# Performance work log

Hardware: AMD Instinct MI355X
Metric: run time of the kernel (lower is better)

The kernel has to match this reference:

```python
import jax, jax.numpy as jnp
import numpy as np

B, PANO, OBJ, CFG, LM, IMG, D = 64, 36, 36, 16, 8, 32, 300
H, EMB, ANG, FEAT = 512, 64, 128, 2176
TOPN = 3
EPS = 1e-8


def setup_inputs() -> dict:
    key = jax.random.key(0)
    ks = jax.random.split(key, 24)
    f = lambda i, shape: jax.random.normal(ks[i], shape, dtype=jnp.float32)
    u = lambda i, shape: jax.random.uniform(ks[i], shape, dtype=jnp.float32)
    s = 0.02
    return {
        "action": f(0, (B, ANG)),
        "feature": f(1, (B, PANO, FEAT)),
        "cand_feat": f(2, (B, IMG, FEAT)),
        "prev_h1": f(3, (B, H)),
        "c_0": f(4, (B, H)),
        "ctx": f(5, (B, CFG, H)),
        "s_0": u(6, (B, CFG)),
        "landmark_object_feature": f(7, (B, CFG, LM, D)),
        "candidate_obj_text_feat": f(8, (B, IMG, OBJ, D)),
        "landmark_mask": u(9, (B, CFG, LM)),
        "landmark_relation": f(10, (B, CFG, LM, 6)),
        "landmark_relation_mask": u(11, (B, CFG, LM)),
        "candidate_relation": f(12, (B, IMG, 6)),
        "pano_obj_feat": f(13, (B, PANO, OBJ, D)),
        "emb_W": f(14, (ANG, EMB)) * s,
        "emb_b": jnp.zeros((EMB,), jnp.float32),
        "W_ih": f(15, (EMB + FEAT + TOPN * D, 4 * H)) * s,
        "W_hh": f(16, (H, 4 * H)) * s,
        "b_lstm": jnp.zeros((4 * H,), jnp.float32),
        "feat_in_W": f(17, (H, FEAT + TOPN * D)) * s,
        "att_in_W": f(18, (H, H)) * s,
        "att_out_W": f(19, (2 * H, H)) * s,
        "cand_in_W": f(20, (H, FEAT + TOPN * 7 + TOPN * D)) * s,
        "ctx_mask": jnp.zeros((B, CFG), dtype=bool),
    }


def _cos_argmax(obj_feat, land_flat):
    # obj_feat: [B,I,O,D], land_flat: [B,M,D] -> argmax over O of cosine sim: [B,I,M]
    dot = jnp.einsum('biod,bmd->biom', obj_feat, land_flat)
    na = jnp.linalg.norm(obj_feat, axis=-1)
    nb = jnp.linalg.norm(land_flat, axis=-1)
    sim = dot / jnp.maximum(na[..., None] * nb[:, None, None, :], EPS)
    return jnp.argmax(sim, axis=2)


def reference(action, feature, cand_feat, prev_h1, c_0, ctx, s_0,
              landmark_object_feature, candidate_obj_text_feat, landmark_mask,
              landmark_relation, landmark_relation_mask, candidate_relation,
              pano_obj_feat, emb_W, emb_b, W_ih, W_hh, b_lstm, feat_in_W,
              att_in_W, att_out_W, cand_in_W, ctx_mask):
    M = CFG * LM
    land_flat = landmark_object_feature.reshape(B, M, D)

    # --- pano object retrieval (cosine argmax + top-N config*landmark gather) ---
    pano_idx = _cos_argmax(pano_obj_feat, land_flat)                   # [B,36,M]
    top_idx = jax.lax.top_k((s_0[..., None] * landmark_mask).reshape(B, M), TOPN)[1]  # [B,3]
    sel = jnp.take_along_axis(pano_idx, jnp.broadcast_to(top_idx[:, None, :], (B, PANO, TOPN)), axis=2)
    pano_sim_obj = jnp.take_along_axis(
        pano_obj_feat, jnp.broadcast_to(sel[..., None], (B, PANO, TOPN, D)), axis=2
    ).reshape(B, PANO, TOPN * D)

    # --- embed action, feature attention (dropout = identity in eval) ---
    action_embeds = jnp.tanh(action @ emb_W + emb_b)
    feat_all = jnp.concatenate([feature, pano_sim_obj], axis=-1)       # [B,36,FEAT+900]
    a = jnp.einsum('bsd,bd->bs', feat_all, prev_h1 @ feat_in_W)
    p = jax.nn.softmax(a, axis=-1)
    attn_feat = jnp.einsum('bs,bsd->bd', p, feat_all)

    # --- LSTM cell ---
    gates = jnp.concatenate([action_embeds, attn_feat], axis=-1) @ W_ih + prev_h1 @ W_hh + b_lstm
    i_g, f_g, g_g, o_g = jnp.split(gates, 4, axis=-1)
    c_1 = jax.nn.sigmoid(f_g) * c_0 + jax.nn.sigmoid(i_g) * jnp.tanh(g_g)
    h_1 = jax.nn.sigmoid(o_g) * jnp.tanh(c_1)

    # --- ctx attention with mask + tilde ---
    lg = jnp.einsum('bsd,bd->bs', ctx, h_1 @ att_in_W)
    lg = jnp.where(ctx_mask, -jnp.inf, lg)
    ctx_attn = jax.nn.softmax(lg, axis=-1)
    wctx = jnp.einsum('bs,bsd->bd', ctx_attn, ctx)
    h_tilde = jnp.tanh(jnp.concatenate([wctx, h_1], axis=-1) @ att_out_W)

    # --- candidate object retrieval ---
    cand_idx = _cos_argmax(candidate_obj_text_feat, land_flat)         # [B,IMG,M]
    ctop = jax.lax.top_k((ctx_attn[..., None] * landmark_mask).reshape(B, M), TOPN)[1]
    land_rel_top = jnp.take_along_axis(landmark_relation.reshape(B, M, 6),
                                       jnp.broadcast_to(ctop[..., None], (B, TOPN, 6)), axis=1)
    land_obj_rel = jnp.einsum('bik,bjk->bij', candidate_relation, land_rel_top)   # [B,IMG,3]
    rel_mask_top = jnp.take_along_axis(landmark_relation_mask.reshape(B, M), ctop, axis=1)  # [B,3]
    csel = jnp.take_along_axis(cand_idx, jnp.broadcast_to(ctop[:, None, :], (B, IMG, TOPN)), axis=2)
    candi_sim_obj = jnp.take_along_axis(
        candidate_obj_text_feat, jnp.broadcast_to(csel[..., None], (B, IMG, TOPN, D)), axis=2)
    candi_rel = candidate_relation[:, :, None, :] * rel_mask_top[:, None, :, None]  # [B,IMG,3,6]
    new_feat = jnp.concatenate(
        [candi_sim_obj, jnp.concatenate([candi_rel, land_obj_rel[..., None]], axis=-1)],
        axis=-1).reshape(B, IMG, TOPN * (D + 7))
    cand_all = jnp.concatenate([cand_feat, new_feat], axis=-1)

    logit = jnp.einsum('bsd,bd->bs', cand_all, h_tilde @ cand_in_W)
    return h_1, c_1, logit, h_tilde, ctx_attn
```

## Files before the change

kernel.cpp:

```cpp
#include <hip/hip_runtime.h>
#include <math.h>

#define B_    64
#define PANO_ 36
#define OBJ_  36
#define CFG_  16
#define LM_   8
#define IMG_  32
#define D_    300
#define H_    512
#define EMB_  64
#define ANG_  128
#define FEAT_ 2176
#define M_    128

__device__ __forceinline__ float sigmoidf(float x) { return 1.0f / (1.0f + expf(-x)); }
__device__ __forceinline__ float dot4(float4 a, float4 b) {
    return a.x * b.x + a.y * b.y + a.z * b.z + a.w * b.w;
}

template <int TWO_SEG>
__global__ __launch_bounds__(256)
void gemm_part(const float* __restrict__ A0, int lda0, int K0, const float* __restrict__ W0,
               const float* __restrict__ A1, int lda1, int K1, const float* __restrict__ W1,
               float* __restrict__ part, int N, int kchunk) {
    __shared__ __align__(16) float As[64][36];
    __shared__ __align__(16) float Bs[32][68];
    const int K = K0 + (TWO_SEG ? K1 : 0);
    int n0 = blockIdx.x * 64;
    int k0 = blockIdx.y * kchunk;
    if (k0 >= K) return;
    int kend = min(K, k0 + kchunk);
    int tid = threadIdx.x;
    int tr = tid >> 4, tc = tid & 15;
    float rA[8], rB[8];
    float acc[4][4] = {};

    auto loadA = [&](int kb) {
#pragma unroll
        for (int l = 0; l < 8; l++) {
            int idx = tid + 256 * l;
            int r = idx >> 5, kk = idx & 31, k = kb + kk;
            float v = 0.f;
            if (k < kend) {
                if (TWO_SEG && k >= K0) v = A1[(size_t)r * lda1 + (k - K0)];
                else                    v = A0[(size_t)r * lda0 + k];
            }
            rA[l] = v;
        }
    };
    auto loadB = [&](int kb) {
#pragma unroll
        for (int l = 0; l < 8; l++) {
            int idx = tid + 256 * l;
            int kk = idx >> 6, c = idx & 63;
            int k = kb + kk, n = n0 + c;
            float v = 0.f;
            if (k < kend && n < N) {
                if (TWO_SEG && k >= K0) v = W1[(size_t)(k - K0) * N + n];
                else                    v = W0[(size_t)k * N + n];
            }
            rB[l] = v;
        }
    };
    auto storeLDS = [&]() {
#pragma unroll
        for (int l = 0; l < 8; l++) {
            int idx = tid + 256 * l;
            As[idx >> 5][idx & 31] = rA[l];
            Bs[idx >> 6][idx & 63] = rB[l];
        }
    };
    auto compute = [&]() {
#pragma unroll
        for (int kk0 = 0; kk0 < 32; kk0 += 4) {
            float4 a0 = *reinterpret_cast<const float4*>(&As[4 * tr + 0][kk0]);
            float4 a1 = *reinterpret_cast<const float4*>(&As[4 * tr + 1][kk0]);
            float4 a2 = *reinterpret_cast<const float4*>(&As[4 * tr + 2][kk0]);
            float4 a3 = *reinterpret_cast<const float4*>(&As[4 * tr + 3][kk0]);
            float4 b0 = *reinterpret_cast<const float4*>(&Bs[kk0 + 0][4 * tc]);
            float4 b1 = *reinterpret_cast<const float4*>(&Bs[kk0 + 1][4 * tc]);
            float4 b2 = *reinterpret_cast<const float4*>(&Bs[kk0 + 2][4 * tc]);
            float4 b3 = *reinterpret_cast<const float4*>(&Bs[kk0 + 3][4 * tc]);
#define ROWFMA(i, ai) \
            acc[i][0] += ai.x * b0.x + ai.y * b1.x + ai.z * b2.x + ai.w * b3.x; \
            acc[i][1] += ai.x * b0.y + ai.y * b1.y + ai.z * b2.y + ai.w * b3.y; \
            acc[i][2] += ai.x * b0.z + ai.y * b1.z + ai.z * b2.z + ai.w * b3.z; \
            acc[i][3] += ai.x * b0.w + ai.y * b1.w + ai.z * b2.w + ai.w * b3.w;
            ROWFMA(0, a0) ROWFMA(1, a1) ROWFMA(2, a2) ROWFMA(3, a3)
#undef ROWFMA
        }
    };

    loadA(k0); loadB(k0);
    storeLDS();
    __syncthreads();
    for (int kb = k0 + 32; kb < kend; kb += 32) {
        loadA(kb); loadB(kb);
        compute();
        __syncthreads();
        storeLDS();
        __syncthreads();
    }
    compute();

    float* outp = part + (size_t)blockIdx.y * 64 * N;
#pragma unroll
    for (int i = 0; i < 4; i++) {
        int r = 4 * tr + i;
#pragma unroll
        for (int j = 0; j < 4; j++) {
            int n = n0 + 4 * tc + j;
            if (n < N) outp[(size_t)r * N + n] = acc[i][j];
        }
    }
}

__global__ void reduce_kernel(const float* __restrict__ part, int S, int total,
                              float* __restrict__ out) {
    int i = blockIdx.x * 256 + threadIdx.x;
    if (i >= total) return;
    float v = 0.f;
    for (int s = 0; s < S; s++) v += part[(size_t)s * total + i];
    out[i] = v;
}

__global__ void reduce_pad_kernel(const float* __restrict__ part, int S, int ncols,
                                  int ostride, float* __restrict__ out) {
    int b = blockIdx.y;
    int i = blockIdx.x * 256 + threadIdx.x;
    if (i >= ncols) return;
    float v = 0.f;
    for (int s = 0; s < S; s++) v += part[(size_t)s * (B_ * ncols) + (size_t)b * ncols + i];
    out[(size_t)b * ostride + i] = v;
}

__global__ void tanh_reduce_kernel(const float* __restrict__ part, int S,
                                   float* __restrict__ htld, float* __restrict__ out_ht) {
    int i = blockIdx.x * 256 + threadIdx.x;
    if (i >= B_ * H_) return;
    float v = 0.f;
    for (int s = 0; s < S; s++) v += part[(size_t)s * (B_ * H_) + i];
    float t = tanhf(v);
    htld[i] = t;
    out_ht[i] = t;
}

__global__ __launch_bounds__(256)
void pano_logits_kernel(const float* __restrict__ pobj,
                        const float* __restrict__ land,
                        const float* __restrict__ s0,
                        const float* __restrict__ lmask,
                        const float* __restrict__ feature,
                        const float* __restrict__ qfeat,
                        int* __restrict__ sel,
                        float* __restrict__ aval) {
    __shared__ __align__(16) float land3[3][304];
    __shared__ int mids[3];
    __shared__ float simv[3][40];
    __shared__ float redV[2];
    __shared__ int redI[2];
    __shared__ int fin[3];
    __shared__ float wred[4];
    int i = blockIdx.x, b = blockIdx.y, tid = threadIdx.x;
    int wave = tid >> 6, lane = tid & 63;

    float tv; int tm;
    if (tid < 128) { tv = s0[b * CFG_ + (tid >> 3)] * lmask[(size_t)b * M_ + tid]; tm = tid; }
    else { tv = -INFINITY; tm = 1 << 30; }
    for (int t = 0; t < 3; t++) {
        float bv = tv; int bi = tm;
        for (int off = 32; off >= 1; off >>= 1) {
            float ov = __shfl_xor(bv, off);
            int   oi = __shfl_xor(bi, off);
            if (ov > bv || (ov == bv && oi < bi)) { bv = ov; bi = oi; }
        }
        if (lane == 0 && wave < 2) { redV[wave] = bv; redI[wave] = bi; }
        __syncthreads();
        if (tid == 0)
            mids[t] = (redV[0] > redV[1] || (redV[0] == redV[1] && redI[0] < redI[1])) ? redI[0] : redI[1];
        __syncthreads();
        if (tm == mids[t]) tv = -INFINITY;
    }

    for (int idx = tid; idx < 912; idx += 256) {
        int t = idx / 304, k = idx % 304;
        land3[t][k] = (k < 300) ? land[((size_t)b * 128 + mids[t]) * 300 + k] : 0.f;
    }
    __syncthreads();

    int g = tid >> 2, gl = tid & 3;
    int o = (g < 36) ? g : 0;
    const float* obase = pobj + (((size_t)b * 36 + i) * 36) * 300;
    const float* row = obase + (size_t)o * 300;
    float c0 = 0, c1 = 0, c2 = 0, sn = 0;
    for (int k4 = gl; k4 < 75; k4 += 4) {
        float4 a  = *reinterpret_cast<const float4*>(row + 4 * k4);
        float4 l0 = *reinterpret_cast<const float4*>(&land3[0][4 * k4]);
        float4 l1 = *reinterpret_cast<const float4*>(&land3[1][4 * k4]);
        float4 l2 = *reinterpret_cast<const float4*>(&land3[2][4 * k4]);
        sn += dot4(a, a);
        c0 += dot4(a, l0);
        c1 += dot4(a, l1);
        c2 += dot4(a, l2);
    }
#pragma unroll
    for (int off = 1; off <= 2; off <<= 1) {
        c0 += __shfl_xor(c0, off);
        c1 += __shfl_xor(c1, off);
        c2 += __shfl_xor(c2, off);
        sn += __shfl_xor(sn, off);
    }
    if (gl == 0 && g < 36) {
        float inv = 1.0f / sqrtf(fmaxf(sn, 1e-20f));
        simv[0][g] = c0 * inv;
        simv[1][g] = c1 * inv;
        simv[2][g] = c2 * inv;
    }
    __syncthreads();
    if (tid < 3) {
        float bv = -INFINITY; int bo = 0;
        for (int o2 = 0; o2 < 36; o2++) {
            float v = simv[tid][o2];
            if (v > bv) { bv = v; bo = o2; }
        }
        fin[tid] = bo;
        sel[((size_t)b * 36 + i) * 3 + tid] = bo;
    }
    __syncthreads();

    const float* qf = qfeat + (size_t)b * 3076;
    const float* frow = feature + ((size_t)b * 36 + i) * 2176;
    float acc = 0;
    for (int d4 = tid; d4 < 544; d4 += 256)
        acc += dot4(*reinterpret_cast<const float4*>(frow + 4 * d4),
                    *reinterpret_cast<const float4*>(qf + 4 * d4));
    for (int idx = tid; idx < 225; idx += 256) {
        int t = idx / 75, k4 = idx % 75;
        acc += dot4(*reinterpret_cast<const float4*>(obase + (size_t)fin[t] * 300 + 4 * k4),
                    *reinterpret_cast<const float4*>(qf + 2176 + t * 300 + 4 * k4));
    }
    for (int off = 32; off >= 1; off >>= 1) acc += __shfl_xor(acc, off);
    if (lane == 0) wred[wave] = acc;
    __syncthreads();
    if (tid == 0) aval[b * 36 + i] = wred[0] + wred[1] + wred[2] + wred[3];
}

__global__ __launch_bounds__(256)
void attn_wsum_kernel(const float* __restrict__ feature,
                      const float* __restrict__ pobj,
                      const int* __restrict__ sel,
                      const float* __restrict__ aval,
                      const float* __restrict__ action,
                      const float* __restrict__ embW,
                      const float* __restrict__ embB,
                      float* __restrict__ xcat) {
    __shared__ float lg[36];
    __shared__ float pe[36];
    __shared__ int ss[36][3];
    int b = blockIdx.y, tid = threadIdx.x;
    int d = blockIdx.x * 256 + tid;
    if (tid < 36) lg[tid] = aval[b * 36 + tid];
    for (int idx = tid; idx < 108; idx += 256) ss[idx / 3][idx % 3] = sel[(size_t)b * 108 + idx];
    __syncthreads();
    float mx = -INFINITY;
    for (int s = 0; s < 36; s++) mx = fmaxf(mx, lg[s]);
    if (tid < 36) pe[tid] = expf(lg[tid] - mx);
    __syncthreads();
    float sum = 0;
    for (int s = 0; s < 36; s++) sum += pe[s];
    float invS = 1.0f / sum;
    if (d < 3076) {
        float acc = 0;
        if (d < 2176) {
            const float* fb = feature + (size_t)b * 36 * 2176 + d;
            for (int s = 0; s < 36; s++) acc += pe[s] * fb[(size_t)s * 2176];
        } else {
            int t = (d - 2176) / 300, k = (d - 2176) % 300;
            const float* pb = pobj + (size_t)b * 36 * 36 * 300;
            for (int s = 0; s < 36; s++)
                acc += pe[s] * pb[((size_t)s * 36 + ss[s][t]) * 300 + k];
        }
        xcat[(size_t)b * 3140 + 64 + d] = acc * invS;
    }
    if (blockIdx.x == 0 && tid < 64) {
        float acc = embB[tid];
        for (int k = 0; k < ANG_; k++)
            acc += action[b * ANG_ + k] * embW[k * EMB_ + tid];
        xcat[(size_t)b * 3140 + tid] = tanhf(acc);
    }
}

__global__ void lstm_kernel(const float* __restrict__ gp, int S,
                            const float* __restrict__ b_lstm,
                            const float* __restrict__ c0,
                            float* __restrict__ out_h1,
                            float* __restrict__ out_c1) {
    int idx = blockIdx.x * 256 + threadIdx.x;
    if (idx >= B_ * H_) return;
    int b = idx >> 9, d = idx & 511;
    float ig = b_lstm[d];
    float fg = b_lstm[512 + d];
    float gg = b_lstm[1024 + d];
    float og = b_lstm[1536 + d];
    for (int s = 0; s < S; s++) {
        const float* g = gp + (size_t)s * (B_ * 2048) + (size_t)b * 2048;
        ig += g[d];
        fg += g[512 + d];
        gg += g[1024 + d];
        og += g[1536 + d];
    }
    float c1 = sigmoidf(fg) * c0[idx] + sigmoidf(ig) * tanhf(gg);
    float h1 = sigmoidf(og) * tanhf(c1);
    out_c1[idx] = c1;
    out_h1[idx] = h1;
}

__global__ __launch_bounds__(256)
void ctx_attn_kernel(const float* __restrict__ ctx,
                     const float* __restrict__ qctx_part,
                     const float* __restrict__ h1f,
                     const float* __restrict__ lmask,
                     float* __restrict__ ccbuf,
                     float* __restrict__ out_attn,
                     int* __restrict__ ctop) {
    __shared__ float qc[512];
    __shared__ float part[16][17];
    __shared__ float lgv[16];
    __shared__ float att[16];
    __shared__ float redV[2];
    __shared__ int redI[2];
    __shared__ int mids[3];
    int b = blockIdx.x, tid = threadIdx.x;
    int wave = tid >> 6, lane = tid & 63;
    for (int idx = tid; idx < 512; idx += 256) {
        float v = 0.f;
#pragma unroll
        for (int s = 0; s < 8; s++) v += qctx_part[(size_t)s * (B_ * 512) + (size_t)b * 512 + idx];
        qc[idx] = v;
    }
    __syncthreads();
    int s = tid >> 4, l = tid & 15;
    float acc = 0;
    for (int d = l; d < 512; d += 16) acc += ctx[((size_t)b * 16 + s) * 512 + d] * qc[d];
    part[s][l] = acc;
    __syncthreads();
    if (tid < 16) {
        float sum = 0;
        for (int j = 0; j < 16; j++) sum += part[tid][j];
        lgv[tid] = sum;
    }
    __syncthreads();
    if (tid < 16) {
        float mx = -INFINITY;
        for (int j = 0; j < 16; j++) mx = fmaxf(mx, lgv[j]);
        att[tid] = expf(lgv[tid] - mx);
    }
    __syncthreads();
    float sum = 0;
    for (int j = 0; j < 16; j++) sum += att[j];
    float invS = 1.0f / sum;
    if (tid < 16) out_attn[b * 16 + tid] = att[tid] * invS;
    for (int d = tid; d < 512; d += 256) {
        float acc2 = 0;
        for (int sj = 0; sj < 16; sj++)
            acc2 += att[sj] * ctx[((size_t)b * 16 + sj) * 512 + d];
        ccbuf[(size_t)b * 1024 + d] = acc2 * invS;
        ccbuf[(size_t)b * 1024 + 512 + d] = h1f[(size_t)b * 512 + d];
    }
    float tv; int tm;
    if (tid < 128) { tv = att[tid >> 3] * lmask[(size_t)b * M_ + tid]; tm = tid; }
    else { tv = -INFINITY; tm = 1 << 30; }
    for (int t = 0; t < 3; t++) {
        float bv = tv; int bi = tm;
        for (int off = 32; off >= 1; off >>= 1) {
            float ov = __shfl_xor(bv, off);
            int   oi = __shfl_xor(bi, off);
            if (ov > bv || (ov == bv && oi < bi)) { bv = ov; bi = oi; }
        }
        if (lane == 0 && wave < 2) { redV[wave] = bv; redI[wave] = bi; }
        __syncthreads();
        if (tid == 0) {
            int pick = (redV[0] > redV[1] || (redV[0] == redV[1] && redI[0] < redI[1])) ? redI[0] : redI[1];
            mids[t] = pick;
            ctop[b * 3 + t] = pick;
        }
        __syncthreads();
        if (tm == mids[t]) tv = -INFINITY;
    }
}

__global__ __launch_bounds__(256)
void cand_fused_kernel(const float* __restrict__ cobj,
                       const float* __restrict__ land,
                       const int* __restrict__ ctop,
                       const float* __restrict__ landrel,
                       const float* __restrict__ lrmask,
                       const float* __restrict__ crel_g,
                       const float* __restrict__ cand_feat,
                       const float* __restrict__ qcand,
                       float* __restrict__ out_logit) {
    __shared__ __align__(16) float land3[3][304];
    __shared__ float relL[3][6];
    __shared__ float relM[3];
    __shared__ float crel[6];
    __shared__ int mids[3];
    __shared__ float simv[3][40];
    __shared__ int fin[3];
    __shared__ float wsum[4];
    int img = blockIdx.x, b = blockIdx.y, tid = threadIdx.x;
    int wave = tid >> 6, lane = tid & 63;
    if (tid < 3) mids[tid] = ctop[b * 3 + tid];
    __syncthreads();
    for (int idx = tid; idx < 912; idx += 256) {
        int t = idx / 304, k = idx % 304;
        land3[t][k] = (k < 300) ? land[((size_t)b * 128 + mids[t]) * 300 + k] : 0.f;
    }
    if (tid < 18) { int t = tid / 6, k = tid % 6; relL[t][k] = landrel[((size_t)b * 128 + mids[t]) * 6 + k]; }
    if (tid >= 32 && tid < 35) { int t = tid - 32; relM[t] = lrmask[(size_t)b * 128 + mids[t]]; }
    if (tid >= 64 && tid < 70) { crel[tid - 64] = crel_g[((size_t)b * 32 + img) * 6 + (tid - 64)]; }
    __syncthreads();

    int g = tid >> 2, gl = tid & 3;
    int o = (g < 36) ? g : 0;
    const float* obase = cobj + (((size_t)b * 32 + img) * 36) * 300;
    const float* row = obase + (size_t)o * 300;
    float c0 = 0, c1 = 0, c2 = 0, sn = 0;
    for (int k4 = gl; k4 < 75; k4 += 4) {
        float4 a  = *reinterpret_cast<const float4*>(row + 4 * k4);
        float4 l0 = *reinterpret_cast<const float4*>(&land3[0][4 * k4]);
        float4 l1 = *reinterpret_cast<const float4*>(&land3[1][4 * k4]);
        float4 l2 = *reinterpret_cast<const float4*>(&land3[2][4 * k4]);
        sn += dot4(a, a);
        c0 += dot4(a, l0);
        c1 += dot4(a, l1);
        c2 += dot4(a, l2);
    }
#pragma unroll
    for (int off = 1; off <= 2; off <<= 1) {
        c0 += __shfl_xor(c0, off);
        c1 += __shfl_xor(c1, off);
        c2 += __shfl_xor(c2, off);
        sn += __shfl_xor(sn, off);
    }
    if (gl == 0 && g < 36) {
        float inv = 1.0f / sqrtf(fmaxf(sn, 1e-20f));
        simv[0][g] = c0 * inv;
        simv[1][g] = c1 * inv;
        simv[2][g] = c2 * inv;
    }
    __syncthreads();
    if (tid < 3) {
        float bv = -INFINITY; int bo = 0;
        for (int o2 = 0; o2 < 36; o2++) {
            float v = simv[tid][o2];
            if (v > bv) { bv = v; bo = o2; }
        }
        fin[tid] = bo;
    }
    __syncthreads();

    const float* q = qcand + (size_t)b * 3104;
    const float* cf = cand_feat + ((size_t)b * 32 + img) * 2176;
    float acc = 0;
    for (int d4 = tid; d4 < 544; d4 += 256)
        acc += dot4(*reinterpret_cast<const float4*>(cf + 4 * d4),
                    *reinterpret_cast<const float4*>(q + 4 * d4));
    for (int idx = tid; idx < 900; idx += 256) {
        int t = idx / 300, k = idx % 300;
        acc += obase[(size_t)fin[t] * 300 + k] * q[2176 + t * 307 + k];
    }
    if (tid < 21) {
        int t = tid / 7, j = tid % 7;
        float val;
        if (j < 6) val = crel[j] * relM[t];
        else { val = 0; for (int k = 0; k < 6; k++) val += crel[k] * relL[t][k]; }
        acc += val * q[2176 + t * 307 + 300 + j];
    }
    for (int off = 32; off >= 1; off >>= 1) acc += __shfl_xor(acc, off);
    if (lane == 0) wsum[wave] = acc;
    __syncthreads();
    if (tid == 0) {
        out_logit[(size_t)b * 32 + img] = wsum[0] + wsum[1] + wsum[2] + wsum[3];
    }
}

extern "C" void kernel_launch(void* const* d_in, const int* in_sizes, int n_in,
                              void* d_out, int out_size, void* d_ws, size_t ws_size,
                              hipStream_t stream) {
    const float* action    = (const float*)d_in[0];
    const float* feature   = (const float*)d_in[1];
    const float* cand_feat = (const float*)d_in[2];
    const float* prev_h1   = (const float*)d_in[3];
    const float* c_0       = (const float*)d_in[4];
    const float* ctx       = (const float*)d_in[5];
    const float* s_0       = (const float*)d_in[6];
    const float* lobj      = (const float*)d_in[7];
    const float* cobj      = (const float*)d_in[8];
    const float* lmask     = (const float*)d_in[9];
    const float* lrel      = (const float*)d_in[10];
    const float* lrelmask  = (const float*)d_in[11];
    const float* crel      = (const float*)d_in[12];
    const float* pobj      = (const float*)d_in[13];
    const float* embW      = (const float*)d_in[14];
    const float* embB      = (const float*)d_in[15];
    const float* W_ih      = (const float*)d_in[16];
    const float* W_hh      = (const float*)d_in[17];
    const float* b_lstm    = (const float*)d_in[18];
    const float* feat_in_W = (const float*)d_in[19];
    const float* att_in_W  = (const float*)d_in[20];
    const float* att_out_W = (const float*)d_in[21];
    const float* cand_in_W = (const float*)d_in[22];

    float* ws = (float*)d_ws;
    float* gates_part = ws;
    float* qf_part    = gates_part + 2621440;
    float* q_feat     = qf_part + 1574912;
    float* qctx_part  = q_feat + 196864;
    float* htpre_part = qctx_part + 262144;
    float* htld       = htpre_part + 524288;
    float* qcand_part = htld + 32768;
    float* q_cand     = qcand_part + 1585664;
    float* xcat       = q_cand + 198656;
    float* ccbuf      = xcat + 200960;
    float* aval       = ccbuf + 65536;
    int*   ctop       = (int*)(aval + 2304);
    int*   sel        = ctop + 192;

    float* out       = (float*)d_out;
    float* out_h1    = out;
    float* out_c1    = out + 32768;
    float* out_logit = out + 65536;
    float* out_ht    = out + 67584;
    float* out_attn  = out + 100352;

    gemm_part<0><<<dim3(49, 8), 256, 0, stream>>>(prev_h1, H_, H_, feat_in_W,
                                                  nullptr, 0, 0, nullptr,
                                                  qf_part, 3076, 64);
    reduce_kernel<<<769, 256, 0, stream>>>(qf_part, 8, 196864, q_feat);

    pano_logits_kernel<<<dim3(PANO_, B_), 256, 0, stream>>>(pobj, lobj, s_0, lmask, feature, q_feat, sel, aval);

    attn_wsum_kernel<<<dim3(13, B_), 256, 0, stream>>>(feature, pobj, sel, aval, action, embW, embB, xcat);

    gemm_part<1><<<dim3(32, 20), 256, 0, stream>>>(xcat, 3140, 3140, W_ih,
                                                   prev_h1, H_, H_, W_hh,
                                                   gates_part, 2048, 192);
    lstm_kernel<<<128, 256, 0, stream>>>(gates_part, 20, b_lstm, c_0, out_h1, out_c1);

    gemm_part<0><<<dim3(8, 8), 256, 0, stream>>>(out_h1, H_, H_, att_in_W,
                                                 nullptr, 0, 0, nullptr,
                                                 qctx_part, H_, 64);
    ctx_attn_kernel<<<B_, 256, 0, stream>>>(ctx, qctx_part, out_h1, lmask, ccbuf, out_attn, ctop);

    gemm_part<0><<<dim3(8, 16), 256, 0, stream>>>(ccbuf, 1024, 1024, att_out_W,
                                                  nullptr, 0, 0, nullptr,
                                                  htpre_part, H_, 64);
    tanh_reduce_kernel<<<128, 256, 0, stream>>>(htpre_part, 16, htld, out_ht);

    gemm_part<0><<<dim3(49, 8), 256, 0, stream>>>(htld, H_, H_, cand_in_W,
                                                  nullptr, 0, 0, nullptr,
                                                  qcand_part, 3097, 64);
    reduce_pad_kernel<<<dim3(13, B_), 256, 0, stream>>>(qcand_part, 8, 3097, 3104, q_cand);

    cand_fused_kernel<<<dim3(IMG_, B_), 256, 0, stream>>>(cobj, lobj, ctop, lrel, lrelmask,
                                                          crel, cand_feat, q_cand, out_logit);
}
```

Before: 462.7 us.

## Vectorize GEMM tile loads, reductions, LSTM and overlap feature dot with cosine pass

Switches the split-K GEMM to float4 global loads and LDS stores for A, and for B when N is a multiple of 4. The reduce, tanh-reduce, LSTM and attention weighted-sum kernels now work on float4 with fewer threads. In pano_logits and cand_fused, 144 threads handle the cosine-similarity rows with a one-step register prefetch while the other 112 threads compute the feature dot product at the same time, instead of doing the two phases one after the other. q_cand is remapped to a 308-stride layout so the selected-object dot can use aligned float4 loads. The intent is to cut the number of memory instructions and hide latency, at the cost of lower thread-level parallelism in some kernels.

```diff
diff --git a/kernel.cpp b/kernel.cpp
--- a/kernel.cpp
+++ b/kernel.cpp
@@ -18,8 +18,15 @@
 __device__ __forceinline__ float dot4(float4 a, float4 b) {
     return a.x * b.x + a.y * b.y + a.z * b.z + a.w * b.w;
 }
-
-template <int TWO_SEG>
+__device__ __forceinline__ float4 add4(float4 a, float4 b) {
+    return make_float4(a.x + b.x, a.y + b.y, a.z + b.z, a.w + b.w);
+}
+__device__ __forceinline__ float4 fma4(float s, float4 a, float4 acc) {
+    return make_float4(acc.x + s * a.x, acc.y + s * a.y, acc.z + s * a.z, acc.w + s * a.w);
+}
+__device__ __forceinline__ float4 ld4(const float* p) { return *reinterpret_cast<const float4*>(p); }
+
+template <int TWO_SEG, int VEC_B>
 __global__ __launch_bounds__(256)
 void gemm_part(const float* __restrict__ A0, int lda0, int K0, const float* __restrict__ W0,
                const float* __restrict__ A1, int lda1, int K1, const float* __restrict__ W1,
@@ -33,55 +40,89 @@
     int kend = min(K, k0 + kchunk);
     int tid = threadIdx.x;
     int tr = tid >> 4, tc = tid & 15;
-    float rA[8], rB[8];
+    float4 rA4[2];
+    float4 rB4[2];
+    float rB[8];
     float acc[4][4] = {};
 
     auto loadA = [&](int kb) {
 #pragma unroll
-        for (int l = 0; l < 8; l++) {
+        for (int l = 0; l < 2; l++) {
             int idx = tid + 256 * l;
-            int r = idx >> 5, kk = idx & 31, k = kb + kk;
-            float v = 0.f;
+            int r = idx >> 3, kq = idx & 7;
+            int k = kb + 4 * kq;
+            float4 v = make_float4(0.f, 0.f, 0.f, 0.f);
             if (k < kend) {
-                if (TWO_SEG && k >= K0) v = A1[(size_t)r * lda1 + (k - K0)];
-                else                    v = A0[(size_t)r * lda0 + k];
+                const float* src = (TWO_SEG && k >= K0)
+                    ? A1 + (size_t)r * lda1 + (k - K0)
+                    : A0 + (size_t)r * lda0 + k;
+                v = ld4(src);
             }
-            rA[l] = v;
+            rA4[l] = v;
         }
     };
     auto loadB = [&](int kb) {
-#pragma unroll
-        for (int l = 0; l < 8; l++) {
-            int idx = tid + 256 * l;
-            int kk = idx >> 6, c = idx & 63;
-            int k = kb + kk, n = n0 + c;
-            float v = 0.f;
-            if (k < kend && n < N) {
-                if (TWO_SEG && k >= K0) v = W1[(size_t)(k - K0) * N + n];
-                else                    v = W0[(size_t)k * N + n];
+        if (VEC_B) {
+#pragma unroll
+            for (int l = 0; l < 2; l++) {
+                int idx = tid + 256 * l;
+                int kk = idx >> 4, c4 = idx & 15;
+                int k = kb + kk, n = n0 + 4 * c4;
+                float4 v = make_float4(0.f, 0.f, 0.f, 0.f);
+                if (k < kend && n < N) {
+                    const float* src = (TWO_SEG && k >= K0)
+                        ? W1 + (size_t)(k - K0) * N + n
+                        : W0 + (size_t)k * N + n;
+                    v = ld4(src);
+                }
+                rB4[l] = v;
             }
-            rB[l] = v;
+        } else {
+#pragma unroll
+            for (int l = 0; l < 8; l++) {
+                int idx = tid + 256 * l;
+                int kk = idx >> 6, c = idx & 63;
+                int k = kb + kk, n = n0 + c;
+                float v = 0.f;
+                if (k < kend && n < N) {
+                    v = (TWO_SEG && k >= K0) ? W1[(size_t)(k - K0) * N + n]
+                                             : W0[(size_t)k * N + n];
+                }
+                rB[l] = v;
+            }
         }
     };
     auto storeLDS = [&]() {
 #pragma unroll
-        for (int l = 0; l < 8; l++) {
+        for (int l = 0; l < 2; l++) {
             int idx = tid + 256 * l;
-            As[idx >> 5][idx & 31] = rA[l];
-            Bs[idx >> 6][idx & 63] = rB[l];
+            *reinterpret_cast<float4*>(&As[idx >> 3][4 * (idx & 7)]) = rA4[l];
+        }
+        if (VEC_B) {
+#pragma unroll
+            for (int l = 0; l < 2; l++) {
+                int idx = tid + 256 * l;
+                *reinterpret_cast<float4*>(&Bs[idx >> 4][4 * (idx & 15)]) = rB4[l];
+            }
+        } else {
+#pragma unroll
+            for (int l = 0; l < 8; l++) {
+                int idx = tid + 256 * l;
+                Bs[idx >> 6][idx & 63] = rB[l];
+            }
         }
     };
     auto compute = [&]() {
 #pragma unroll
         for (int kk0 = 0; kk0 < 32; kk0 += 4) {
-            float4 a0 = *reinterpret_cast<const float4*>(&As[4 * tr + 0][kk0]);
-            float4 a1 = *reinterpret_cast<const float4*>(&As[4 * tr + 1][kk0]);
-            float4 a2 = *reinterpret_cast<const float4*>(&As[4 * tr + 2][kk0]);
-            float4 a3 = *reinterpret_cast<const float4*>(&As[4 * tr + 3][kk0]);
-            float4 b0 = *reinterpret_cast<const float4*>(&Bs[kk0 + 0][4 * tc]);
-            float4 b1 = *reinterpret_cast<const float4*>(&Bs[kk0 + 1][4 * tc]);
-            float4 b2 = *reinterpret_cast<const float4*>(&Bs[kk0 + 2][4 * tc]);
-            float4 b3 = *reinterpret_cast<const float4*>(&Bs[kk0 + 3][4 * tc]);
+            float4 a0 = ld4(&As[4 * tr + 0][kk0]);
+            float4 a1 = ld4(&As[4 * tr + 1][kk0]);
+            float4 a2 = ld4(&As[4 * tr + 2][kk0]);
+            float4 a3 = ld4(&As[4 * tr + 3][kk0]);
+            float4 b0 = ld4(&Bs[kk0 + 0][4 * tc]);
+            float4 b1 = ld4(&Bs[kk0 + 1][4 * tc]);
+            float4 b2 = ld4(&Bs[kk0 + 2][4 * tc]);
+            float4 b3 = ld4(&Bs[kk0 + 3][4 * tc]);
 #define ROWFMA(i, ai) \
             acc[i][0] += ai.x * b0.x + ai.y * b1.x + ai.z * b2.x + ai.w * b3.x; \
             acc[i][1] += ai.x * b0.y + ai.y * b1.y + ai.z * b2.y + ai.w * b3.y; \
@@ -105,43 +146,57 @@
     compute();
 
     float* outp = part + (size_t)blockIdx.y * 64 * N;
-#pragma unroll
-    for (int i = 0; i < 4; i++) {
-        int r = 4 * tr + i;
-#pragma unroll
-        for (int j = 0; j < 4; j++) {
-            int n = n0 + 4 * tc + j;
-            if (n < N) outp[(size_t)r * N + n] = acc[i][j];
-        }
-    }
-}
-
-__global__ void reduce_kernel(const float* __restrict__ part, int S, int total,
-                              float* __restrict__ out) {
+    if (VEC_B) {
+#pragma unroll
+        for (int i = 0; i < 4; i++) {
+            int r = 4 * tr + i;
+            int n = n0 + 4 * tc;
+            if (n < N)
+                *reinterpret_cast<float4*>(outp + (size_t)r * N + n) =
+                    make_float4(acc[i][0], acc[i][1], acc[i][2], acc[i][3]);
+        }
+    } else {
+#pragma unroll
+        for (int i = 0; i < 4; i++) {
+            int r = 4 * tr + i;
+#pragma unroll
+            for (int j = 0; j < 4; j++) {
+                int n = n0 + 4 * tc + j;
+                if (n < N) outp[(size_t)r * N + n] = acc[i][j];
+            }
+        }
+    }
+}
+
+__global__ void reduce4_kernel(const float4* __restrict__ part, int S, int total4,
+                               float4* __restrict__ out) {
     int i = blockIdx.x * 256 + threadIdx.x;
-    if (i >= total) return;
+    if (i >= total4) return;
+    float4 v = make_float4(0.f, 0.f, 0.f, 0.f);
+    for (int s = 0; s < S; s++) v = add4(v, part[(size_t)s * total4 + i]);
+    out[i] = v;
+}
+
+__global__ void reduce_remap_kernel(const float* __restrict__ part, int S,
+                                    float* __restrict__ out) {
+    int b = blockIdx.y;
+    int c = blockIdx.x * 256 + threadIdx.x;
+    if (c >= 3097) return;
     float v = 0.f;
-    for (int s = 0; s < S; s++) v += part[(size_t)s * total + i];
-    out[i] = v;
-}
-
-__global__ void reduce_pad_kernel(const float* __restrict__ part, int S, int ncols,
-                                  int ostride, float* __restrict__ out) {
-    int b = blockIdx.y;
+    for (int s = 0; s < S; s++) v += part[(size_t)s * (B_ * 3097) + (size_t)b * 3097 + c];
+    int oc;
+    if (c < 2176) oc = c;
+    else { int u = c - 2176; oc = 2176 + (u / 307) * 308 + (u % 307); }
+    out[(size_t)b * 3104 + oc] = v;
+}
+
+__global__ void tanh_reduce_kernel(const float4* __restrict__ part, int S,
+                                   float4* __restrict__ htld, float4* __restrict__ out_ht) {
     int i = blockIdx.x * 256 + threadIdx.x;
-    if (i >= ncols) return;
-    float v = 0.f;
-    for (int s = 0; s < S; s++) v += part[(size_t)s * (B_ * ncols) + (size_t)b * ncols + i];
-    out[(size_t)b * ostride + i] = v;
-}
-
-__global__ void tanh_reduce_kernel(const float* __restrict__ part, int S,
-                                   float* __restrict__ htld, float* __restrict__ out_ht) {
-    int i = blockIdx.x * 256 + threadIdx.x;
-    if (i >= B_ * H_) return;
-    float v = 0.f;
-    for (int s = 0; s < S; s++) v += part[(size_t)s * (B_ * H_) + i];
-    float t = tanhf(v);
+    if (i >= B_ * H_ / 4) return;
+    float4 v = make_float4(0.f, 0.f, 0.f, 0.f);
+    for (int s = 0; s < S; s++) v = add4(v, part[(size_t)s * (B_ * H_ / 4) + i]);
+    float4 t = make_float4(tanhf(v.x), tanhf(v.y), tanhf(v.z), tanhf(v.w));
     htld[i] = t;
     out_ht[i] = t;
 }
@@ -189,33 +244,44 @@
     }
     __syncthreads();
 
-    int g = tid >> 2, gl = tid & 3;
-    int o = (g < 36) ? g : 0;
     const float* obase = pobj + (((size_t)b * 36 + i) * 36) * 300;
-    const float* row = obase + (size_t)o * 300;
-    float c0 = 0, c1 = 0, c2 = 0, sn = 0;
-    for (int k4 = gl; k4 < 75; k4 += 4) {
-        float4 a  = *reinterpret_cast<const float4*>(row + 4 * k4);
-        float4 l0 = *reinterpret_cast<const float4*>(&land3[0][4 * k4]);
-        float4 l1 = *reinterpret_cast<const float4*>(&land3[1][4 * k4]);
-        float4 l2 = *reinterpret_cast<const float4*>(&land3[2][4 * k4]);
-        sn += dot4(a, a);
-        c0 += dot4(a, l0);
-        c1 += dot4(a, l1);
-        c2 += dot4(a, l2);
-    }
-#pragma unroll
-    for (int off = 1; off <= 2; off <<= 1) {
-        c0 += __shfl_xor(c0, off);
-        c1 += __shfl_xor(c1, off);
-        c2 += __shfl_xor(c2, off);
-        sn += __shfl_xor(sn, off);
-    }
-    if (gl == 0 && g < 36) {
-        float inv = 1.0f / sqrtf(fmaxf(sn, 1e-20f));
-        simv[0][g] = c0 * inv;
-        simv[1][g] = c1 * inv;
-        simv[2][g] = c2 * inv;
+    const float* qf = qfeat + (size_t)b * 3076;
+    const float* frow = feature + ((size_t)b * 36 + i) * 2176;
+    float facc = 0.f;
+
+    if (tid < 144) {
+        int g = tid >> 2, gl = tid & 3;
+        const float* row = obase + (size_t)g * 300;
+        float c0 = 0, c1 = 0, c2 = 0, sn = 0;
+        float4 a = ld4(row + 4 * gl);
+        for (int k4 = gl; k4 < 75; k4 += 4) {
+            float4 cur = a;
+            int kn = k4 + 4;
+            if (kn < 75) a = ld4(row + 4 * kn);
+            float4 l0 = ld4(&land3[0][4 * k4]);
+            float4 l1 = ld4(&land3[1][4 * k4]);
+            float4 l2 = ld4(&land3[2][4 * k4]);
+            sn += dot4(cur, cur);
+            c0 += dot4(cur, l0);
+            c1 += dot4(cur, l1);
+            c2 += dot4(cur, l2);
+        }
+#pragma unroll
+        for (int off = 1; off <= 2; off <<= 1) {
+            c0 += __shfl_xor(c0, off);
+            c1 += __shfl_xor(c1, off);
+            c2 += __shfl_xor(c2, off);
+            sn += __shfl_xor(sn, off);
+        }
+        if (gl == 0) {
+            float inv = 1.0f / sqrtf(fmaxf(sn, 1e-20f));
+            simv[0][g] = c0 * inv;
+            simv[1][g] = c1 * inv;
+            simv[2][g] = c2 * inv;
+        }
+    } else {
+        for (int d4 = tid - 144; d4 < 544; d4 += 112)
+            facc += dot4(ld4(frow + 4 * d4), ld4(qf + 4 * d4));
     }
     __syncthreads();
     if (tid < 3) {
@@ -229,16 +295,11 @@
     }
     __syncthreads();
 
-    const float* qf = qfeat + (size_t)b * 3076;
-    const float* frow = feature + ((size_t)b * 36 + i) * 2176;
-    float acc = 0;
-    for (int d4 = tid; d4 < 544; d4 += 256)
-        acc += dot4(*reinterpret_cast<const float4*>(frow + 4 * d4),
-                    *reinterpret_cast<const float4*>(qf + 4 * d4));
+    float acc = facc;
     for (int idx = tid; idx < 225; idx += 256) {
         int t = idx / 75, k4 = idx % 75;
-        acc += dot4(*reinterpret_cast<const float4*>(obase + (size_t)fin[t] * 300 + 4 * k4),
-                    *reinterpret_cast<const float4*>(qf + 2176 + t * 300 + 4 * k4));
+        acc += dot4(ld4(obase + (size_t)fin[t] * 300 + 4 * k4),
+                    ld4(qf + 2176 + t * 300 + 4 * k4));
     }
     for (int off = 32; off >= 1; off >>= 1) acc += __shfl_xor(acc, off);
     if (lane == 0) wred[wave] = acc;
@@ -259,7 +320,7 @@
     __shared__ float pe[36];
     __shared__ int ss[36][3];
     int b = blockIdx.y, tid = threadIdx.x;
-    int d = blockIdx.x * 256 + tid;
+    int d4 = blockIdx.x * 256 + tid;
     if (tid < 36) lg[tid] = aval[b * 36 + tid];
     for (int idx = tid; idx < 108; idx += 256) ss[idx / 3][idx % 3] = sel[(size_t)b * 108 + idx];
     __syncthreads();
@@ -270,18 +331,19 @@
     float sum = 0;
     for (int s = 0; s < 36; s++) sum += pe[s];
     float invS = 1.0f / sum;
-    if (d < 3076) {
-        float acc = 0;
-        if (d < 2176) {
-            const float* fb = feature + (size_t)b * 36 * 2176 + d;
-            for (int s = 0; s < 36; s++) acc += pe[s] * fb[(size_t)s * 2176];
+    if (d4 < 769) {
+        float4 acc = make_float4(0.f, 0.f, 0.f, 0.f);
+        if (d4 < 544) {
+            const float* fb = feature + (size_t)b * 36 * 2176 + 4 * d4;
+            for (int s = 0; s < 36; s++) acc = fma4(pe[s], ld4(fb + (size_t)s * 2176), acc);
         } else {
-            int t = (d - 2176) / 300, k = (d - 2176) % 300;
+            int u = d4 - 544, t = u / 75, k4 = u % 75;
             const float* pb = pobj + (size_t)b * 36 * 36 * 300;
             for (int s = 0; s < 36; s++)
-                acc += pe[s] * pb[((size_t)s * 36 + ss[s][t]) * 300 + k];
-        }
-        xcat[(size_t)b * 3140 + 64 + d] = acc * invS;
+                acc = fma4(pe[s], ld4(pb + ((size_t)s * 36 + ss[s][t]) * 300 + 4 * k4), acc);
+        }
+        acc = make_float4(acc.x * invS, acc.y * invS, acc.z * invS, acc.w * invS);
+        *reinterpret_cast<float4*>(xcat + (size_t)b * 3140 + 64 + 4 * d4) = acc;
     }
     if (blockIdx.x == 0 && tid < 64) {
         float acc = embB[tid];
@@ -296,24 +358,33 @@
                             const float* __restrict__ c0,
                             float* __restrict__ out_h1,
                             float* __restrict__ out_c1) {
-    int idx = blockIdx.x * 256 + threadIdx.x;
-    if (idx >= B_ * H_) return;
-    int b = idx >> 9, d = idx & 511;
-    float ig = b_lstm[d];
-    float fg = b_lstm[512 + d];
-    float gg = b_lstm[1024 + d];
-    float og = b_lstm[1536 + d];
+    int idx4 = blockIdx.x * 256 + threadIdx.x;
+    if (idx4 >= B_ * H_ / 4) return;
+    int b = idx4 >> 7;
+    int d4 = idx4 & 127;
+    float4 ig = ld4(b_lstm + 4 * d4);
+    float4 fg = ld4(b_lstm + 512 + 4 * d4);
+    float4 gg = ld4(b_lstm + 1024 + 4 * d4);
+    float4 og = ld4(b_lstm + 1536 + 4 * d4);
     for (int s = 0; s < S; s++) {
-        const float* g = gp + (size_t)s * (B_ * 2048) + (size_t)b * 2048;
-        ig += g[d];
-        fg += g[512 + d];
-        gg += g[1024 + d];
-        og += g[1536 + d];
-    }
-    float c1 = sigmoidf(fg) * c0[idx] + sigmoidf(ig) * tanhf(gg);
-    float h1 = sigmoidf(og) * tanhf(c1);
-    out_c1[idx] = c1;
-    out_h1[idx] = h1;
+        const float* g = gp + (size_t)s * (B_ * 2048) + (size_t)b * 2048 + 4 * d4;
+        ig = add4(ig, ld4(g));
+        fg = add4(fg, ld4(g + 512));
+        gg = add4(gg, ld4(g + 1024));
+        og = add4(og, ld4(g + 1536));
+    }
+    float4 cv = ld4(c0 + 4 * idx4);
+    float4 c1, h1;
+    c1.x = sigmoidf(fg.x) * cv.x + sigmoidf(ig.x) * tanhf(gg.x);
+    c1.y = sigmoidf(fg.y) * cv.y + sigmoidf(ig.y) * tanhf(gg.y);
+    c1.z = sigmoidf(fg.z) * cv.z + sigmoidf(ig.z) * tanhf(gg.z);
+    c1.w = sigmoidf(fg.w) * cv.w + sigmoidf(ig.w) * tanhf(gg.w);
+    h1.x = sigmoidf(og.x) * tanhf(c1.x);
+    h1.y = sigmoidf(og.y) * tanhf(c1.y);
+    h1.z = sigmoidf(og.z) * tanhf(c1.z);
+    h1.w = sigmoidf(og.w) * tanhf(c1.w);
+    *reinterpret_cast<float4*>(out_c1 + 4 * idx4) = c1;
+    *reinterpret_cast<float4*>(out_h1 + 4 * idx4) = h1;
 }
 
 __global__ __launch_bounds__(256)
@@ -324,7 +395,7 @@
                      float* __restrict__ ccbuf,
                      float* __restrict__ out_attn,
                      int* __restrict__ ctop) {
-    __shared__ float qc[512];
+    __shared__ __align__(16) float qc[512];
     __shared__ float part[16][17];
     __shared__ float lgv[16];
     __shared__ float att[16];
@@ -333,11 +404,12 @@
     __shared__ int mids[3];
     int b = blockIdx.x, tid = threadIdx.x;
     int wave = tid >> 6, lane = tid & 63;
-    for (int idx = tid; idx < 512; idx += 256) {
-        float v = 0.f;
-#pragma unroll
-        for (int s = 0; s < 8; s++) v += qctx_part[(size_t)s * (B_ * 512) + (size_t)b * 512 + idx];
-        qc[idx] = v;
+    if (tid < 128) {
+        float4 v = make_float4(0.f, 0.f, 0.f, 0.f);
+#pragma unroll
+        for (int s = 0; s < 8; s++)
+            v = add4(v, ld4(qctx_part + (size_t)s * (B_ * 512) + (size_t)b * 512 + 4 * tid));
+        *reinterpret_cast<float4*>(&qc[4 * tid]) = v;
     }
     __syncthreads();
     int s = tid >> 4, l = tid & 15;
@@ -421,33 +493,44 @@
     if (tid >= 64 && tid < 70) { crel[tid - 64] = crel_g[((size_t)b * 32 + img) * 6 + (tid - 64)]; }
     __syncthreads();
 
-    int g = tid >> 2, gl = tid & 3;
-    int o = (g < 36) ? g : 0;
     const float* obase = cobj + (((size_t)b * 32 + img) * 36) * 300;
-    const float* row = obase + (size_t)o * 300;
-    float c0 = 0, c1 = 0, c2 = 0, sn = 0;
-    for (int k4 = gl; k4 < 75; k4 += 4) {
-        float4 a  = *reinterpret_cast<const float4*>(row + 4 * k4);
-        float4 l0 = *reinterpret_cast<const float4*>(&land3[0][4 * k4]);
-        float4 l1 = *reinterpret_cast<const float4*>(&land3[1][4 * k4]);
-        float4 l2 = *reinterpret_cast<const float4*>(&land3[2][4 * k4]);
-        sn += dot4(a, a);
-        c0 += dot4(a, l0);
-        c1 += dot4(a, l1);
-        c2 += dot4(a, l2);
-    }
-#pragma unroll
-    for (int off = 1; off <= 2; off <<= 1) {
-        c0 += __shfl_xor(c0, off);
-        c1 += __shfl_xor(c1, off);
-        c2 += __shfl_xor(c2, off);
-        sn += __shfl_xor(sn, off);
-    }
-    if (gl == 0 && g < 36) {
-        float inv = 1.0f / sqrtf(fmaxf(sn, 1e-20f));
-        simv[0][g] = c0 * inv;
-        simv[1][g] = c1 * inv;
-        simv[2][g] = c2 * inv;
+    const float* q = qcand + (size_t)b * 3104;
+    const float* cf = cand_feat + ((size_t)b * 32 + img) * 2176;
+    float facc = 0.f;
+
+    if (tid < 144) {
+        int g = tid >> 2, gl = tid & 3;
+        const float* row = obase + (size_t)g * 300;
+        float c0 = 0, c1 = 0, c2 = 0, sn = 0;
+        float4 a = ld4(row + 4 * gl);
+        for (int k4 = gl; k4 < 75; k4 += 4) {
+            float4 cur = a;
+            int kn = k4 + 4;
+            if (kn < 75) a = ld4(row + 4 * kn);
+            float4 l0 = ld4(&land3[0][4 * k4]);
+            float4 l1 = ld4(&land3[1][4 * k4]);
+            float4 l2 = ld4(&land3[2][4 * k4]);
+            sn += dot4(cur, cur);
+            c0 += dot4(cur, l0);
+            c1 += dot4(cur, l1);
+            c2 += dot4(cur, l2);
+        }
+#pragma unroll
+        for (int off = 1; off <= 2; off <<= 1) {
+            c0 += __shfl_xor(c0, off);
+            c1 += __shfl_xor(c1, off);
+            c2 += __shfl_xor(c2, off);
+            sn += __shfl_xor(sn, off);
+        }
+        if (gl == 0) {
+            float inv = 1.0f / sqrtf(fmaxf(sn, 1e-20f));
+            simv[0][g] = c0 * inv;
+            simv[1][g] = c1 * inv;
+            simv[2][g] = c2 * inv;
+        }
+    } else {
+        for (int d4 = tid - 144; d4 < 544; d4 += 112)
+            facc += dot4(ld4(cf + 4 * d4), ld4(q + 4 * d4));
     }
     __syncthreads();
     if (tid < 3) {
@@ -460,22 +543,18 @@
     }
     __syncthreads();
 
-    const float* q = qcand + (size_t)b * 3104;
-    const float* cf = cand_feat + ((size_t)b * 32 + img) * 2176;
-    float acc = 0;
-    for (int d4 = tid; d4 < 544; d4 += 256)
-        acc += dot4(*reinterpret_cast<const float4*>(cf + 4 * d4),
-                    *reinterpret_cast<const float4*>(q + 4 * d4));
-    for (int idx = tid; idx < 900; idx += 256) {
-        int t = idx / 300, k = idx % 300;
-        acc += obase[(size_t)fin[t] * 300 + k] * q[2176 + t * 307 + k];
+    float acc = facc;
+    for (int idx = tid; idx < 225; idx += 256) {
+        int t = idx / 75, k4 = idx % 75;
+        acc += dot4(ld4(obase + (size_t)fin[t] * 300 + 4 * k4),
+                    ld4(q + 2176 + t * 308 + 4 * k4));
     }
     if (tid < 21) {
         int t = tid / 7, j = tid % 7;
         float val;
         if (j < 6) val = crel[j] * relM[t];
         else { val = 0; for (int k = 0; k < 6; k++) val += crel[k] * relL[t][k]; }
-        acc += val * q[2176 + t * 307 + 300 + j];
+        acc += val * q[2176 + t * 308 + 300 + j];
     }
     for (int off = 32; off >= 1; off >>= 1) acc += __shfl_xor(acc, off);
     if (lane == 0) wsum[wave] = acc;
@@ -534,34 +613,35 @@
     float* out_ht    = out + 67584;
     float* out_attn  = out + 100352;
 
-    gemm_part<0><<<dim3(49, 8), 256, 0, stream>>>(prev_h1, H_, H_, feat_in_W,
-                                                  nullptr, 0, 0, nullptr,
-                                                  qf_part, 3076, 64);
-    reduce_kernel<<<769, 256, 0, stream>>>(qf_part, 8, 196864, q_feat);
+    gemm_part<0, 1><<<dim3(49, 8), 256, 0, stream>>>(prev_h1, H_, H_, feat_in_W,
+                                                     nullptr, 0, 0, nullptr,
+                                                     qf_part, 3076, 64);
+    reduce4_kernel<<<193, 256, 0, stream>>>((const float4*)qf_part, 8, 49216, (float4*)q_feat);
 
     pano_logits_kernel<<<dim3(PANO_, B_), 256, 0, stream>>>(pobj, lobj, s_0, lmask, feature, q_feat, sel, aval);
 
-    attn_wsum_kernel<<<dim3(13, B_), 256, 0, stream>>>(feature, pobj, sel, aval, action, embW, embB, xcat);
-
-    gemm_part<1><<<dim3(32, 20), 256, 0, stream>>>(xcat, 3140, 3140, W_ih,
-                                                   prev_h1, H_, H_, W_hh,
-                                                   gates_part, 2048, 192);
-    lstm_kernel<<<128, 256, 0, stream>>>(gates_part, 20, b_lstm, c_0, out_h1, out_c1);
-
-    gemm_part<0><<<dim3(8, 8), 256, 0, stream>>>(out_h1, H_, H_, att_in_W,
-                                                 nullptr, 0, 0, nullptr,
-                                                 qctx_part, H_, 64);
+    attn_wsum_kernel<<<dim3(4, B_), 256, 0, stream>>>(feature, pobj, sel, aval, action, embW, embB, xcat);
+
+    gemm_part<1, 1><<<dim3(32, 20), 256, 0, stream>>>(xcat, 3140, 3140, W_ih,
+                                                      prev_h1, H_, H_, W_hh,
+                                                      gates_part, 2048, 192);
+    lstm_kernel<<<32, 256, 0, stream>>>(gates_part, 20, b_lstm, c_0, out_h1, out_c1);
+
+    gemm_part<0, 1><<<dim3(8, 8), 256, 0, stream>>>(out_h1, H_, H_, att_in_W,
+                                                    nullptr, 0, 0, nullptr,
+                                                    qctx_part, H_, 64);
     ctx_attn_kernel<<<B_, 256, 0, stream>>>(ctx, qctx_part, out_h1, lmask, ccbuf, out_attn, ctop);
 
-    gemm_part<0><<<dim3(8, 16), 256, 0, stream>>>(ccbuf, 1024, 1024, att_out_W,
-                                                  nullptr, 0, 0, nullptr,
-                                                  htpre_part, H_, 64);
-    tanh_reduce_kernel<<<128, 256, 0, stream>>>(htpre_part, 16, htld, out_ht);
-
-    gemm_part<0><<<dim3(49, 8), 256, 0, stream>>>(htld, H_, H_, cand_in_W,
-                                                  nullptr, 0, 0, nullptr,
-                                                  qcand_part, 3097, 64);
-    reduce_pad_kernel<<<dim3(13, B_), 256, 0, stream>>>(qcand_part, 8, 3097, 3104, q_cand);
+    gemm_part<0, 1><<<dim3(8, 16), 256, 0, stream>>>(ccbuf, 1024, 1024, att_out_W,
+                                                     nullptr, 0, 0, nullptr,
+                                                     htpre_part, H_, 64);
+    tanh_reduce_kernel<<<32, 256, 0, stream>>>((const float4*)htpre_part, 16,
+                                               (float4*)htld, (float4*)out_ht);
+
+    gemm_part<0, 0><<<dim3(49, 8), 256, 0, stream>>>(htld, H_, H_, cand_in_W,
+                                                     nullptr, 0, 0, nullptr,
+                                                     qcand_part, 3097, 64);
+    reduce_remap_kernel<<<dim3(13, B_), 256, 0, stream>>>(qcand_part, 8, q_cand);
 
     cand_fused_kernel<<<dim3(IMG_, B_), 256, 0, stream>>>(cobj, lobj, ctop, lrel, lrelmask,
                                                           crel, cand_feat, q_cand, out_logit);
```

Measured after the change: 449.0 us. 3.0% less time.
